# Kernel optimization log

Hardware: AMD Instinct MI355X
Metric: run time of the kernel (lower is better)

Reference implementation:

```python
import jax, jax.numpy as jnp
import numpy as np

B, L, R, D, K, H = 512, 10, 2048, 256, 20, 128
VOCAB, GEO_V, GEO_D = 30000, 1000, 64

def _l2norm(x):
    # F.normalize(p=2, dim=-1): x / max(||x||, eps)
    return x / jnp.maximum(jnp.linalg.norm(x, axis=-1, keepdims=True), 1e-12)

def setup_inputs() -> dict:
    key = jax.random.key(0)
    ks = jax.random.split(key, 20)
    emb = 0.02 * jax.random.normal(ks[0], (VOCAB, D), jnp.float32)
    emb = emb.at[0].set(0.0)  # padding_idx=0 row is zero
    inp = {
        'text_left': jax.random.randint(ks[1], (B, L), 0, VOCAB),
        'text_right': jax.random.randint(ks[2], (B, R), 0, VOCAB),
        'location_left': jax.random.randint(ks[3], (B, 2), 0, GEO_V),
        'distance': jax.random.uniform(ks[4], (B,), jnp.float32),
        'emb': emb,
        'attn_w': 0.05 * jax.random.normal(ks[5], (D,), jnp.float32),
        'w_m0': 0.1 * jax.random.normal(ks[6], (K, H), jnp.float32),
        'b_m0': jnp.zeros((H,), jnp.float32),
        'w_m1': 0.1 * jax.random.normal(ks[7], (H, H), jnp.float32),
        'b_m1': jnp.zeros((H,), jnp.float32),
        'w_m2': 0.1 * jax.random.normal(ks[8], (H, 1), jnp.float32),
        'b_m2': jnp.zeros((1,), jnp.float32),
        'out_w': 0.5 * jax.random.normal(ks[9], (1, 1), jnp.float32),
        'out_b': jnp.zeros((1,), jnp.float32),
        'lat_tab': 0.05 * jax.random.normal(ks[10], (GEO_V, GEO_D), jnp.float32),
        'lon_tab': 0.05 * jax.random.normal(ks[11], (GEO_V, GEO_D), jnp.float32),
        'w3': 0.05 * jax.random.normal(ks[12], (D, 10), jnp.float32),
        'b3': jnp.zeros((10,), jnp.float32),
        'w5': 0.05 * jax.random.normal(ks[13], (GEO_D, 32), jnp.float32),
        'b5': jnp.zeros((32,), jnp.float32),
        'w4': 0.05 * jax.random.normal(ks[14], (164, 2), jnp.float32),
        'b4': jnp.zeros((2,), jnp.float32),
    }
    return inp

def reference(text_left, text_right, location_left, distance, emb, attn_w,
              w_m0, b_m0, w_m1, b_m1, w_m2, b_m2, out_w, out_b,
              lat_tab, lon_tab, w3, b3, w5, b5, w4, b4):
    # ---- no_grad block in the original ----
    mask_query = text_left == 0  # mask_value = 0
    embed_query = emb[text_left]            # [B,L,D]
    embed_doc = emb[text_right]             # [B,R,D]
    matching = jnp.einsum('bld,brd->blr', _l2norm(embed_query), _l2norm(embed_doc))
    topk = jax.lax.top_k(matching, K)[0]    # [B,L,K], sorted descending
    logits = jnp.einsum('bld,d->bl', embed_query, attn_w)
    logits = jnp.where(mask_query, -jnp.inf, logits)
    attn = jax.nn.softmax(logits, axis=-1)  # [B,L]
    h = jnp.tanh(topk @ w_m0 + b_m0)
    h = jnp.tanh(h @ w_m1 + b_m1)
    h = jnp.tanh(h @ w_m2 + b_m2)[..., 0]   # [B,L]
    x = jnp.einsum('bl,bl->b', h, attn)[:, None]  # [B,1]
    x = jnp.tanh(x @ out_w + out_b)         # out layer (tanh)
    x = jax.lax.stop_gradient(x)
    embed_query = jax.lax.stop_gradient(embed_query)
    # ---- trainable geo/weighting branch ----
    lat = lat_tab[location_left[:, 0]] @ w5 + b5   # [B,32]
    lon = lon_tab[location_left[:, 1]] @ w5 + b5   # [B,32]
    q1 = (embed_query @ w3 + b3).reshape(embed_query.shape[0], -1)  # [B,100]
    w = jnp.concatenate([q1, lat, lon], axis=-1) @ w4 + b4          # [B,2]
    x_all = jnp.concatenate([x, distance[:, None]], axis=1)         # [B,2]
    pred = jnp.sum(w * x_all, axis=1, keepdims=True)                # [B,1]
    return pred
```

## Files before the change

### kernel.cpp

```cpp
#include <hip/hip_runtime.h>
#include <hip/hip_fp16.h>
#include <math.h>

#define BB 512
#define LL 10
#define RR 2048
#define DD 256
#define KK 20
#define HH 128
#define NVOCAB 30000
#define GEOD 64

#define FP8_SCALE   64.0f
#define FP8_DESCALE (1.0f / 4096.0f)

#define EMB8_BYTES (NVOCAB * DD)
#define BLOB1_OFF  EMB8_BYTES
#define BLOB2_OFF  (BLOB1_OFF + 8192)
#define W3T_OFF    (BLOB2_OFF + 32768)
#define W5T_OFF    (W3T_OFF + 10240)

typedef __attribute__((ext_vector_type(2))) long long llx2;
typedef __attribute__((ext_vector_type(4))) float f32x4;
typedef __attribute__((ext_vector_type(8))) short bf16x8;

static __device__ inline unsigned short f2bf(float f) {
    unsigned u = __float_as_uint(f);
    unsigned r = (u + 0x7fff + ((u >> 16) & 1)) >> 16;
    return (unsigned short)r;
}

__global__ __launch_bounds__(256) void pre_kernel(
    const float* __restrict__ emb,
    const float* __restrict__ w_m0, const float* __restrict__ w_m1,
    const float* __restrict__ w3,   const float* __restrict__ w5,
    unsigned char* __restrict__ emb8,
    unsigned short* __restrict__ blob1, unsigned short* __restrict__ blob2,
    float* __restrict__ w3T, float* __restrict__ w5T)
{
    if (blockIdx.x < 7500) {
        int row  = blockIdx.x * 4 + (threadIdx.x >> 6);
        int lane = threadIdx.x & 63;
        int e0 = ((lane >> 1) & 7) * 32 + (lane >> 4) * 8 + (lane & 1) * 4;
        float4 v = *(const float4*)(emb + (size_t)row * DD + e0);
        float ssq = v.x * v.x + v.y * v.y + v.z * v.z + v.w * v.w;
        #pragma unroll
        for (int off = 32; off; off >>= 1) ssq += __shfl_xor(ssq, off);
        float s = FP8_SCALE / fmaxf(sqrtf(ssq), 1e-12f);
        unsigned pk = 0;
        pk = (unsigned)__builtin_amdgcn_cvt_pk_fp8_f32(v.x * s, v.y * s, (int)pk, false);
        pk = (unsigned)__builtin_amdgcn_cvt_pk_fp8_f32(v.z * s, v.w * s, (int)pk, true);
        ((unsigned*)(emb8 + (size_t)row * DD))[lane] = pk;
    } else {
        int i = (blockIdx.x - 7500) * 256 + threadIdx.x;
        if (i < 4096) {
            int t = i >> 9, ln = (i >> 3) & 63, tt = i & 7;
            int n = t * 16 + (ln & 15), k = (ln >> 4) * 8 + tt;
            blob1[i] = (k < KK) ? f2bf(w_m0[k * HH + n]) : (unsigned short)0;
        } else if (i < 4096 + 16384) {
            int i2 = i - 4096;
            int ks = i2 >> 12, rem = i2 & 4095;
            int t = rem >> 9, ln = (rem >> 3) & 63, tt = rem & 7;
            int n = t * 16 + (ln & 15), k = ks * 32 + (ln >> 4) * 8 + tt;
            blob2[i2] = f2bf(w_m1[k * HH + n]);
        } else if (i < 4096 + 16384 + 2560) {
            int i3 = i - (4096 + 16384);
            int j = i3 >> 8, d = i3 & 255;
            w3T[i3] = w3[d * 10 + j];
        } else if (i < 4096 + 16384 + 2560 + 2048) {
            int i4 = i - (4096 + 16384 + 2560);
            int c = i4 >> 6, d = i4 & 63;
            w5T[i4] = w5[d * 32 + c];
        }
    }
}

static __device__ inline unsigned wave_umax_u32(unsigned x)
{
    unsigned t;
    t = (unsigned)__builtin_amdgcn_update_dpp((int)x, (int)x, 0x111, 0xF, 0xF, false); x = x > t ? x : t;
    t = (unsigned)__builtin_amdgcn_update_dpp((int)x, (int)x, 0x112, 0xF, 0xF, false); x = x > t ? x : t;
    t = (unsigned)__builtin_amdgcn_update_dpp((int)x, (int)x, 0x114, 0xF, 0xF, false); x = x > t ? x : t;
    t = (unsigned)__builtin_amdgcn_update_dpp((int)x, (int)x, 0x118, 0xF, 0xF, false); x = x > t ? x : t;
    t = (unsigned)__builtin_amdgcn_update_dpp((int)x, (int)x, 0x142, 0xF, 0xF, false); x = x > t ? x : t;
    t = (unsigned)__builtin_amdgcn_update_dpp((int)x, (int)x, 0x143, 0xF, 0xF, false); x = x > t ? x : t;
    return (unsigned)__builtin_amdgcn_readlane((int)x, 63);
}

static __device__ inline void build_top2(const unsigned short* __restrict__ row,
                                         int lane, unsigned extmask,
                                         unsigned& k1, unsigned& k2)
{
    unsigned m1 = 0u, m2 = 0u;
    #pragma unroll
    for (int k = 0; k < 32; ++k) {
        int j = lane + 64 * k;
        unsigned key = ((unsigned)row[j] << 16) | (unsigned)(2047 - j);
        key = ((extmask >> k) & 1u) ? 0u : key;
        unsigned mn = m1 < key ? m1 : key;
        m1 = m1 > key ? m1 : key;
        m2 = m2 > mn ? m2 : mn;
    }
    k1 = m1; k2 = m2;
}

__global__ __launch_bounds__(512, 4) void fused_kernel(
    const int*   __restrict__ text_left,
    const int*   __restrict__ text_right,
    const int*   __restrict__ loc_left,
    const float* __restrict__ distance,
    const float* __restrict__ emb,
    const float* __restrict__ attn_w,
    const float* __restrict__ b_m0, const float* __restrict__ b_m1,
    const float* __restrict__ w_m2, const float* __restrict__ b_m2,
    const float* __restrict__ out_w, const float* __restrict__ out_b,
    const float* __restrict__ lat_tab, const float* __restrict__ lon_tab,
    const float* __restrict__ b3, const float* __restrict__ b5,
    const float* __restrict__ w4, const float* __restrict__ b4,
    const unsigned char*  __restrict__ emb8,
    const unsigned short* __restrict__ blob1,
    const unsigned short* __restrict__ blob2,
    const float* __restrict__ w3T, const float* __restrict__ w5T,
    float*       __restrict__ out)
{
    __shared__ __align__(16) unsigned char arena[32768];
    __shared__ __align__(16) unsigned short s_keys[LL][RR];
    __shared__ float s_logit[LL];
    __shared__ float s_h[16];
    __shared__ float s_feat[164];

    unsigned short* s_h1   = (unsigned short*)arena;
    float*          s_topk = (float*)(arena + 4096);

    const int b    = blockIdx.x;
    const int tid  = threadIdx.x;
    const int lane = tid & 63;
    const int wid  = tid >> 6;
    const int m15  = lane & 15, q = lane >> 4;

    {
        llx2 afr[4];
        {
            int qidx = (m15 < LL) ? text_left[b * LL + m15] : 0;
            const unsigned char* ap = emb8 + (size_t)qidx * DD + q * 64;
            #pragma unroll
            for (int s = 0; s < 4; ++s) afr[s] = *(const llx2*)(ap + s * 16);
        }
        const int* trb = text_right + b * RR;
        const int T0 = wid * 16;
        const int r0 = lane >> 4;
        const int c  = lane & 15;

        unsigned char* stg = arena + wid * 4096;

        int  I[4];
        llx2 R[4];

        auto LOADI = [&](int t) {
            const int* p = trb + (T0 + t) * 16 + r0;
            I[0] = p[0]; I[1] = p[4]; I[2] = p[8]; I[3] = p[12];
        };
        auto LOADR = [&]() {
            #pragma unroll
            for (int j = 0; j < 4; ++j)
                R[j] = *(const llx2*)(emb8 + (size_t)I[j] * DD + (c << 4));
        };
        auto STORE = [&]() {
            #pragma unroll
            for (int j = 0; j < 4; ++j) {
                int r = j * 4 + r0;
                *(llx2*)(stg + r * 256 + ((c ^ r) << 4)) = R[j];
            }
        };
        auto COMPUTE = [&](int t) {
            llx2 bf[4];
            #pragma unroll
            for (int s = 0; s < 4; ++s)
                bf[s] = *(const llx2*)(stg + m15 * 256 + (((q * 4 + s) ^ m15) << 4));
            f32x4 acc = {0.f, 0.f, 0.f, 0.f};
            #pragma unroll
            for (int s = 0; s < 4; ++s) {
                acc = __builtin_amdgcn_mfma_f32_16x16x32_fp8_fp8(afr[s][0], bf[s][0], acc, 0, 0, 0);
                acc = __builtin_amdgcn_mfma_f32_16x16x32_fp8_fp8(afr[s][1], bf[s][1], acc, 0, 0, 0);
            }
            int n0 = (T0 + t) * 16;
            #pragma unroll
            for (int v = 0; v < 4; ++v) {
                int m = q * 4 + v;
                if (m < LL) {
                    float sc = acc[v] * FP8_DESCALE;
                    unsigned hb = (unsigned)__half_as_ushort(__float2half(sc));
                    unsigned ok = hb ^ ((hb & 0x8000u) ? 0xFFFFu : 0x8000u);
                    s_keys[m][n0 + m15] = (unsigned short)ok;
                }
            }
        };

        LOADI(0); LOADR(); LOADI(1);
        #pragma unroll 1
        for (int t = 0; t < 16; ++t) {
            STORE();
            if (t < 15) {
                LOADR();
                if (t < 14) LOADI(t + 2);
            }
            COMPUTE(t);
        }
    }
    __syncthreads();

    {
        int row = tid >> 5, col = tid & 31;
        if (row >= LL || col >= KK) s_topk[row * 32 + col] = 0.f;
    }

    {
        auto TOPK_ROW = [&](int l) {
            const unsigned short* krow = &s_keys[l][0];
            unsigned extmask = 0u, k1, k2;
            build_top2(krow, lane, extmask, k1, k2);
            #pragma unroll 1
            for (int it = 0; it < KK; ++it) {
                unsigned bmk = wave_umax_u32(k1);
                if (k1 == bmk) {
                    unsigned o16 = bmk >> 16;
                    unsigned hbv = (o16 & 0x8000u) ? (o16 & 0x7FFFu) : (o16 ^ 0xFFFFu);
                    s_topk[l * 32 + it] = __half2float(__ushort_as_half((unsigned short)hbv));
                    int j = 2047 - (int)(bmk & 0xFFFFu);
                    extmask |= 1u << (j >> 6);
                    k1 = k2; k2 = 0u;
                }
                if (__any(k1 == 0u)) {
                    if (k1 == 0u) build_top2(krow, lane, extmask, k1, k2);
                }
            }
        };
        TOPK_ROW(wid);
        if (wid >= 6) {
            TOPK_ROW(wid + 2);
        } else if (wid == 4) {
            const float4 aw = *(const float4*)(attn_w + lane * 4);
            for (int l = 0; l < LL; ++l) {
                int v = text_left[b * LL + l];
                float4 qv = *(const float4*)(emb + (size_t)v * DD + lane * 4);
                float d = qv.x * aw.x + qv.y * aw.y + qv.z * aw.z + qv.w * aw.w;
                #pragma unroll
                for (int off = 32; off; off >>= 1) d += __shfl_xor(d, off);
                if (lane == 0) s_logit[l] = (v == 0) ? -INFINITY : d;
            }
        } else if (wid == 5) {
            int c = lane & 31, which = lane >> 5;
            int v = loc_left[b * 2 + which];
            const float* tab = which ? lon_tab : lat_tab;
            const float4* tr = (const float4*)(tab + (size_t)v * GEOD);
            const float4* wr = (const float4*)(w5T + c * GEOD);
            float a = b5[c];
            #pragma unroll
            for (int d4 = 0; d4 < 16; ++d4) {
                float4 tv = tr[d4], wv = wr[d4];
                a += tv.x * wv.x + tv.y * wv.y + tv.z * wv.z + tv.w * wv.w;
            }
            s_feat[100 + which * 32 + c] = a;
        } else if (wid == 2 || wid == 3) {
            int p = (wid - 2) * 64 + lane;
            if (p < 100) {
                int l = p / 10, j = p % 10;
                int v = text_left[b * LL + l];
                const float4* qr = (const float4*)(emb + (size_t)v * DD);
                const float4* wr = (const float4*)(w3T + j * DD);
                float a = b3[j];
                #pragma unroll 8
                for (int d4 = 0; d4 < 64; ++d4) {
                    float4 qv = qr[d4], wv = wr[d4];
                    a += qv.x * wv.x + qv.y * wv.y + qv.z * wv.z + qv.w * wv.w;
                }
                s_feat[p] = a;
            }
        }
    }
    __syncthreads();

    if (wid == 0) {
        float tv[8];
        *(float4*)(tv)     = *(const float4*)(&s_topk[m15 * 32 + q * 8]);
        *(float4*)(tv + 4) = *(const float4*)(&s_topk[m15 * 32 + q * 8 + 4]);
        bf16x8 a1;
        #pragma unroll
        for (int t = 0; t < 8; ++t) a1[t] = (short)f2bf(tv[t]);
        f32x4 acc1[8];
        #pragma unroll
        for (int t = 0; t < 8; ++t) {
            bf16x8 b1 = *(const bf16x8*)(blob1 + t * 512 + lane * 8);
            f32x4 z = {0.f, 0.f, 0.f, 0.f};
            acc1[t] = __builtin_amdgcn_mfma_f32_16x16x32_bf16(a1, b1, z, 0, 0, 0);
        }
        #pragma unroll
        for (int t = 0; t < 8; ++t) {
            int c = t * 16 + m15;
            float bb0 = b_m0[c];
            #pragma unroll
            for (int v = 0; v < 4; ++v) {
                int m = q * 4 + v;
                float h = tanhf(acc1[t][v] + bb0);
                s_h1[m * 128 + (((c >> 3) ^ m) << 3) + (c & 7)] = f2bf(h);
            }
        }
        f32x4 acc2[8];
        #pragma unroll
        for (int t = 0; t < 8; ++t) acc2[t] = (f32x4){0.f, 0.f, 0.f, 0.f};
        #pragma unroll
        for (int ks = 0; ks < 4; ++ks) {
            bf16x8 a2 = *(const bf16x8*)(s_h1 + m15 * 128 + (((ks * 4 + q) ^ m15) << 3));
            #pragma unroll
            for (int t = 0; t < 8; ++t) {
                bf16x8 b2 = *(const bf16x8*)(blob2 + (ks * 8 + t) * 512 + lane * 8);
                acc2[t] = __builtin_amdgcn_mfma_f32_16x16x32_bf16(a2, b2, acc2[t], 0, 0, 0);
            }
        }
        float part[4] = {0.f, 0.f, 0.f, 0.f};
        #pragma unroll
        for (int t = 0; t < 8; ++t) {
            int c = t * 16 + m15;
            float bb1 = b_m1[c];
            float wm2 = w_m2[c];
            #pragma unroll
            for (int v = 0; v < 4; ++v)
                part[v] += tanhf(acc2[t][v] + bb1) * wm2;
        }
        #pragma unroll
        for (int v = 0; v < 4; ++v) {
            #pragma unroll
            for (int off = 1; off < 16; off <<= 1) part[v] += __shfl_xor(part[v], off);
        }
        if (m15 == 0) {
            #pragma unroll
            for (int v = 0; v < 4; ++v) {
                int m = q * 4 + v;
                if (m < LL) s_h[m] = tanhf(part[v] + b_m2[0]);
            }
        }
        float w0p = 0.f, w1p = 0.f;
        #pragma unroll
        for (int i = lane; i < 164; i += 64) {
            float f = s_feat[i];
            w0p += f * w4[i * 2 + 0];
            w1p += f * w4[i * 2 + 1];
        }
        #pragma unroll
        for (int off = 32; off; off >>= 1) {
            w0p += __shfl_xor(w0p, off);
            w1p += __shfl_xor(w1p, off);
        }
        if (lane == 0) {
            float mx = -INFINITY;
            #pragma unroll
            for (int l = 0; l < LL; ++l) mx = fmaxf(mx, s_logit[l]);
            float ex[LL];
            float sum = 0.f;
            #pragma unroll
            for (int l = 0; l < LL; ++l) { ex[l] = expf(s_logit[l] - mx); sum += ex[l]; }
            float x = 0.f;
            #pragma unroll
            for (int l = 0; l < LL; ++l) x += s_h[l] * (ex[l] / sum);
            float xo = tanhf(x * out_w[0] + out_b[0]);
            out[b] = (w0p + b4[0]) * xo + (w1p + b4[1]) * distance[b];
        }
    }
}

extern "C" void kernel_launch(void* const* d_in, const int* in_sizes, int n_in,
                              void* d_out, int out_size, void* d_ws, size_t ws_size,
                              hipStream_t stream) {
    const int*   text_left  = (const int*)  d_in[0];
    const int*   text_right = (const int*)  d_in[1];
    const int*   loc_left   = (const int*)  d_in[2];
    const float* distance   = (const float*)d_in[3];
    const float* emb        = (const float*)d_in[4];
    const float* attn_w     = (const float*)d_in[5];
    const float* w_m0       = (const float*)d_in[6];
    const float* b_m0       = (const float*)d_in[7];
    const float* w_m1       = (const float*)d_in[8];
    const float* b_m1       = (const float*)d_in[9];
    const float* w_m2       = (const float*)d_in[10];
    const float* b_m2       = (const float*)d_in[11];
    const float* out_w      = (const float*)d_in[12];
    const float* out_b      = (const float*)d_in[13];
    const float* lat_tab    = (const float*)d_in[14];
    const float* lon_tab    = (const float*)d_in[15];
    const float* w3         = (const float*)d_in[16];
    const float* b3         = (const float*)d_in[17];
    const float* w5         = (const float*)d_in[18];
    const float* b5         = (const float*)d_in[19];
    const float* w4         = (const float*)d_in[20];
    const float* b4         = (const float*)d_in[21];

    unsigned char*  ws    = (unsigned char*)d_ws;
    unsigned char*  emb8  = ws;
    unsigned short* blob1 = (unsigned short*)(ws + BLOB1_OFF);
    unsigned short* blob2 = (unsigned short*)(ws + BLOB2_OFF);
    float*          w3T   = (float*)(ws + W3T_OFF);
    float*          w5T   = (float*)(ws + W5T_OFF);
    float*          out   = (float*)d_out;

    pre_kernel<<<7598, 256, 0, stream>>>(emb, w_m0, w_m1, w3, w5,
                                         emb8, blob1, blob2, w3T, w5T);

    fused_kernel<<<BB, 512, 0, stream>>>(
        text_left, text_right, loc_left, distance, emb, attn_w,
        b_m0, b_m1, w_m2, b_m2, out_w, out_b,
        lat_tab, lon_tab, b3, b5, w4, b4,
        emb8, blob1, blob2, w3T, w5T, out);
}
```

Baseline: 57.58 us.

## Replace shared-memory key buffer with register-resident hierarchical top-k merge

Each wave now keeps its match scores in registers and tracks a running top-2 per row while computing. It then extracts a local top-20 per 16-lane group using shuffles, and a second stage merges 8x20 candidates per row from a small shared buffer. This removes the 40KB s_keys shared array and the full 2048-wide rescans, which should cut LDS traffic and raise occupancy. In exchange it uses more registers (savek, k1/k2 arrays) and adds an extra merge stage, and the side-branch work is redistributed across waves.

```diff
diff --git a/kernel.cpp b/kernel.cpp
--- a/kernel.cpp
+++ b/kernel.cpp
@@ -87,21 +87,14 @@
     return (unsigned)__builtin_amdgcn_readlane((int)x, 63);
 }
 
-static __device__ inline void build_top2(const unsigned short* __restrict__ row,
-                                         int lane, unsigned extmask,
-                                         unsigned& k1, unsigned& k2)
+static __device__ inline unsigned grp16_umax(unsigned x)
 {
-    unsigned m1 = 0u, m2 = 0u;
-    #pragma unroll
-    for (int k = 0; k < 32; ++k) {
-        int j = lane + 64 * k;
-        unsigned key = ((unsigned)row[j] << 16) | (unsigned)(2047 - j);
-        key = ((extmask >> k) & 1u) ? 0u : key;
-        unsigned mn = m1 < key ? m1 : key;
-        m1 = m1 > key ? m1 : key;
-        m2 = m2 > mn ? m2 : mn;
-    }
-    k1 = m1; k2 = m2;
+    unsigned t;
+    t = (unsigned)__shfl_xor((int)x, 1); x = x > t ? x : t;
+    t = (unsigned)__shfl_xor((int)x, 2); x = x > t ? x : t;
+    t = (unsigned)__shfl_xor((int)x, 4); x = x > t ? x : t;
+    t = (unsigned)__shfl_xor((int)x, 8); x = x > t ? x : t;
+    return x;
 }
 
 __global__ __launch_bounds__(512, 4) void fused_kernel(
@@ -124,13 +117,12 @@
     float*       __restrict__ out)
 {
     __shared__ __align__(16) unsigned char arena[32768];
-    __shared__ __align__(16) unsigned short s_keys[LL][RR];
+    __shared__ unsigned s_merge[LL][160];
+    __shared__ __align__(16) float s_topkf[16 * 32];
+    __shared__ __align__(16) unsigned short s_h1[16 * 128];
     __shared__ float s_logit[LL];
     __shared__ float s_h[16];
     __shared__ float s_feat[164];
-
-    unsigned short* s_h1   = (unsigned short*)arena;
-    float*          s_topk = (float*)(arena + 4096);
 
     const int b    = blockIdx.x;
     const int tid  = threadIdx.x;
@@ -138,6 +130,10 @@
     const int wid  = tid >> 6;
     const int m15  = lane & 15, q = lane >> 4;
 
+    unsigned savek[4][8];
+    unsigned k1[4] = {0u, 0u, 0u, 0u};
+    unsigned k2[4] = {0u, 0u, 0u, 0u};
+    const int T0 = wid * 16;
     {
         llx2 afr[4];
         {
@@ -147,10 +143,8 @@
             for (int s = 0; s < 4; ++s) afr[s] = *(const llx2*)(ap + s * 16);
         }
         const int* trb = text_right + b * RR;
-        const int T0 = wid * 16;
         const int r0 = lane >> 4;
         const int c  = lane & 15;
-
         unsigned char* stg = arena + wid * 4096;
 
         int  I[4];
@@ -172,118 +166,166 @@
                 *(llx2*)(stg + r * 256 + ((c ^ r) << 4)) = R[j];
             }
         };
-        auto COMPUTE = [&](int t) {
-            llx2 bf[4];
-            #pragma unroll
-            for (int s = 0; s < 4; ++s)
-                bf[s] = *(const llx2*)(stg + m15 * 256 + (((q * 4 + s) ^ m15) << 4));
-            f32x4 acc = {0.f, 0.f, 0.f, 0.f};
-            #pragma unroll
-            for (int s = 0; s < 4; ++s) {
-                acc = __builtin_amdgcn_mfma_f32_16x16x32_fp8_fp8(afr[s][0], bf[s][0], acc, 0, 0, 0);
-                acc = __builtin_amdgcn_mfma_f32_16x16x32_fp8_fp8(afr[s][1], bf[s][1], acc, 0, 0, 0);
-            }
-            int n0 = (T0 + t) * 16;
-            #pragma unroll
-            for (int v = 0; v < 4; ++v) {
-                int m = q * 4 + v;
-                if (m < LL) {
-                    float sc = acc[v] * FP8_DESCALE;
-                    unsigned hb = (unsigned)__half_as_ushort(__float2half(sc));
-                    unsigned ok = hb ^ ((hb & 0x8000u) ? 0xFFFFu : 0x8000u);
-                    s_keys[m][n0 + m15] = (unsigned short)ok;
+
+#define COMPT(T) { \
+        llx2 bf0 = *(const llx2*)(stg + m15 * 256 + (((q * 4 + 0) ^ m15) << 4)); \
+        llx2 bf1 = *(const llx2*)(stg + m15 * 256 + (((q * 4 + 1) ^ m15) << 4)); \
+        llx2 bf2 = *(const llx2*)(stg + m15 * 256 + (((q * 4 + 2) ^ m15) << 4)); \
+        llx2 bf3 = *(const llx2*)(stg + m15 * 256 + (((q * 4 + 3) ^ m15) << 4)); \
+        f32x4 acc = {0.f, 0.f, 0.f, 0.f}; \
+        acc = __builtin_amdgcn_mfma_f32_16x16x32_fp8_fp8(afr[0][0], bf0[0], acc, 0, 0, 0); \
+        acc = __builtin_amdgcn_mfma_f32_16x16x32_fp8_fp8(afr[0][1], bf0[1], acc, 0, 0, 0); \
+        acc = __builtin_amdgcn_mfma_f32_16x16x32_fp8_fp8(afr[1][0], bf1[0], acc, 0, 0, 0); \
+        acc = __builtin_amdgcn_mfma_f32_16x16x32_fp8_fp8(afr[1][1], bf1[1], acc, 0, 0, 0); \
+        acc = __builtin_amdgcn_mfma_f32_16x16x32_fp8_fp8(afr[2][0], bf2[0], acc, 0, 0, 0); \
+        acc = __builtin_amdgcn_mfma_f32_16x16x32_fp8_fp8(afr[2][1], bf2[1], acc, 0, 0, 0); \
+        acc = __builtin_amdgcn_mfma_f32_16x16x32_fp8_fp8(afr[3][0], bf3[0], acc, 0, 0, 0); \
+        acc = __builtin_amdgcn_mfma_f32_16x16x32_fp8_fp8(afr[3][1], bf3[1], acc, 0, 0, 0); \
+        _Pragma("unroll") \
+        for (int v = 0; v < 4; ++v) { \
+            float sc_ = acc[v] * FP8_DESCALE; \
+            unsigned hb_ = (unsigned)__half_as_ushort(__float2half(sc_)); \
+            unsigned ok_ = hb_ ^ ((hb_ & 0x8000u) ? 0xFFFFu : 0x8000u); \
+            if ((T) & 1) savek[v][(T) >> 1] |= ok_ << 16; \
+            else         savek[v][(T) >> 1]  = ok_; \
+            unsigned key_ = (ok_ << 16) | (2047u - (unsigned)(((T0 + (T)) << 4) + m15)); \
+            key_ = ((q * 4 + v) < LL) ? key_ : 0u; \
+            unsigned mn_ = k1[v] < key_ ? k1[v] : key_; \
+            k1[v] = k1[v] > key_ ? k1[v] : key_; \
+            k2[v] = k2[v] > mn_ ? k2[v] : mn_; \
+        } }
+
+#define TILE(T) { STORE(); if ((T) < 15) { LOADR(); } if ((T) < 14) { LOADI((T) + 2); } COMPT(T); }
+
+        LOADI(0); LOADR(); LOADI(1);
+        TILE(0)  TILE(1)  TILE(2)  TILE(3)
+        TILE(4)  TILE(5)  TILE(6)  TILE(7)
+        TILE(8)  TILE(9)  TILE(10) TILE(11)
+        TILE(12) TILE(13) TILE(14) TILE(15)
+#undef TILE
+#undef COMPT
+    }
+
+    {
+        #pragma unroll
+        for (int v = 0; v < 4; ++v) {
+            const int m = q * 4 + v;
+            if (m < LL) {
+                unsigned k1v = k1[v], k2v = k2[v];
+                unsigned last = 0xFFFFFFFFu;
+                #pragma unroll 1
+                for (int it = 0; it < KK; ++it) {
+                    unsigned bmk = grp16_umax(k1v);
+                    if (k1v == bmk) {
+                        s_merge[m][wid * 20 + it] = bmk;
+                        k1v = k2v; k2v = 0u;
+                    }
+                    last = bmk;
+                    if (k1v == 0u) {
+                        unsigned m1 = 0u, m2 = 0u;
+                        #pragma unroll
+                        for (int t = 0; t < 16; ++t) {
+                            unsigned ok = (t & 1) ? (savek[v][t >> 1] >> 16)
+                                                  : (savek[v][t >> 1] & 0xFFFFu);
+                            unsigned key = (ok << 16) | (2047u - (unsigned)(((T0 + t) << 4) + m15));
+                            key = (key < last) ? key : 0u;
+                            unsigned mn = m1 < key ? m1 : key;
+                            m1 = m1 > key ? m1 : key;
+                            m2 = m2 > mn ? m2 : mn;
+                        }
+                        k1v = m1; k2v = m2;
+                    }
                 }
             }
-        };
-
-        LOADI(0); LOADR(); LOADI(1);
-        #pragma unroll 1
-        for (int t = 0; t < 16; ++t) {
-            STORE();
-            if (t < 15) {
-                LOADR();
-                if (t < 14) LOADI(t + 2);
-            }
-            COMPUTE(t);
         }
     }
     __syncthreads();
 
     {
         int row = tid >> 5, col = tid & 31;
-        if (row >= LL || col >= KK) s_topk[row * 32 + col] = 0.f;
-    }
-
-    {
-        auto TOPK_ROW = [&](int l) {
-            const unsigned short* krow = &s_keys[l][0];
-            unsigned extmask = 0u, k1, k2;
-            build_top2(krow, lane, extmask, k1, k2);
+        if (row >= LL || col >= KK) s_topkf[row * 32 + col] = 0.f;
+    }
+    if (wid < 5) {
+        #pragma unroll 1
+        for (int rr = 0; rr < 2; ++rr) {
+            int m = wid + rr * 5;
+            unsigned s0 = s_merge[m][lane];
+            unsigned s1 = s_merge[m][lane + 64];
+            unsigned s2 = (lane < 32) ? s_merge[m][lane + 128] : 0u;
+            unsigned m1 = s0 > s1 ? s0 : s1;
+            unsigned m2 = s0 > s1 ? s1 : s0;
+            unsigned mn = m1 < s2 ? m1 : s2;
+            m1 = m1 > s2 ? m1 : s2;
+            m2 = m2 > mn ? m2 : mn;
+            unsigned last = 0xFFFFFFFFu;
             #pragma unroll 1
             for (int it = 0; it < KK; ++it) {
-                unsigned bmk = wave_umax_u32(k1);
-                if (k1 == bmk) {
+                unsigned bmk = wave_umax_u32(m1);
+                if (m1 == bmk) {
                     unsigned o16 = bmk >> 16;
                     unsigned hbv = (o16 & 0x8000u) ? (o16 & 0x7FFFu) : (o16 ^ 0xFFFFu);
-                    s_topk[l * 32 + it] = __half2float(__ushort_as_half((unsigned short)hbv));
-                    int j = 2047 - (int)(bmk & 0xFFFFu);
-                    extmask |= 1u << (j >> 6);
-                    k1 = k2; k2 = 0u;
+                    s_topkf[m * 32 + it] = __half2float(__ushort_as_half((unsigned short)hbv));
+                    m1 = m2; m2 = 0u;
                 }
-                if (__any(k1 == 0u)) {
-                    if (k1 == 0u) build_top2(krow, lane, extmask, k1, k2);
+                last = bmk;
+                if (__any(m1 == 0u)) {
+                    if (m1 == 0u) {
+                        unsigned a0 = (s0 < last) ? s0 : 0u;
+                        unsigned a1 = (s1 < last) ? s1 : 0u;
+                        unsigned a2 = (s2 < last) ? s2 : 0u;
+                        m1 = a0 > a1 ? a0 : a1;
+                        m2 = a0 > a1 ? a1 : a0;
+                        unsigned mn2 = m1 < a2 ? m1 : a2;
+                        m1 = m1 > a2 ? m1 : a2;
+                        m2 = m2 > mn2 ? m2 : mn2;
+                    }
                 }
             }
-        };
-        TOPK_ROW(wid);
-        if (wid >= 6) {
-            TOPK_ROW(wid + 2);
-        } else if (wid == 4) {
-            const float4 aw = *(const float4*)(attn_w + lane * 4);
-            for (int l = 0; l < LL; ++l) {
-                int v = text_left[b * LL + l];
-                float4 qv = *(const float4*)(emb + (size_t)v * DD + lane * 4);
-                float d = qv.x * aw.x + qv.y * aw.y + qv.z * aw.z + qv.w * aw.w;
-                #pragma unroll
-                for (int off = 32; off; off >>= 1) d += __shfl_xor(d, off);
-                if (lane == 0) s_logit[l] = (v == 0) ? -INFINITY : d;
-            }
-        } else if (wid == 5) {
-            int c = lane & 31, which = lane >> 5;
-            int v = loc_left[b * 2 + which];
-            const float* tab = which ? lon_tab : lat_tab;
-            const float4* tr = (const float4*)(tab + (size_t)v * GEOD);
-            const float4* wr = (const float4*)(w5T + c * GEOD);
-            float a = b5[c];
-            #pragma unroll
-            for (int d4 = 0; d4 < 16; ++d4) {
-                float4 tv = tr[d4], wv = wr[d4];
-                a += tv.x * wv.x + tv.y * wv.y + tv.z * wv.z + tv.w * wv.w;
-            }
-            s_feat[100 + which * 32 + c] = a;
-        } else if (wid == 2 || wid == 3) {
-            int p = (wid - 2) * 64 + lane;
-            if (p < 100) {
-                int l = p / 10, j = p % 10;
-                int v = text_left[b * LL + l];
-                const float4* qr = (const float4*)(emb + (size_t)v * DD);
-                const float4* wr = (const float4*)(w3T + j * DD);
-                float a = b3[j];
-                #pragma unroll 8
-                for (int d4 = 0; d4 < 64; ++d4) {
-                    float4 qv = qr[d4], wv = wr[d4];
-                    a += qv.x * wv.x + qv.y * wv.y + qv.z * wv.z + qv.w * wv.w;
-                }
-                s_feat[p] = a;
-            }
+        }
+    } else if (wid == 5) {
+        const float4 aw = *(const float4*)(attn_w + lane * 4);
+        for (int l = 0; l < LL; ++l) {
+            int v = text_left[b * LL + l];
+            float4 qv = *(const float4*)(emb + (size_t)v * DD + lane * 4);
+            float d = qv.x * aw.x + qv.y * aw.y + qv.z * aw.z + qv.w * aw.w;
+            #pragma unroll
+            for (int off = 32; off; off >>= 1) d += __shfl_xor(d, off);
+            if (lane == 0) s_logit[l] = (v == 0) ? -INFINITY : d;
+        }
+        int c = lane & 31, which = lane >> 5;
+        int v = loc_left[b * 2 + which];
+        const float* tab = which ? lon_tab : lat_tab;
+        const float4* tr = (const float4*)(tab + (size_t)v * GEOD);
+        const float4* wr = (const float4*)(w5T + c * GEOD);
+        float a = b5[c];
+        #pragma unroll
+        for (int d4 = 0; d4 < 16; ++d4) {
+            float4 tv = tr[d4], wv = wr[d4];
+            a += tv.x * wv.x + tv.y * wv.y + tv.z * wv.z + tv.w * wv.w;
+        }
+        s_feat[100 + which * 32 + c] = a;
+    } else {
+        int p = (wid - 6) * 64 + lane;
+        if (p < 100) {
+            int l = p / 10, j = p % 10;
+            int v = text_left[b * LL + l];
+            const float4* qr = (const float4*)(emb + (size_t)v * DD);
+            const float4* wr = (const float4*)(w3T + j * DD);
+            float a = b3[j];
+            #pragma unroll 8
+            for (int d4 = 0; d4 < 64; ++d4) {
+                float4 qv = qr[d4], wv = wr[d4];
+                a += qv.x * wv.x + qv.y * wv.y + qv.z * wv.z + qv.w * wv.w;
+            }
+            s_feat[p] = a;
         }
     }
     __syncthreads();
 
     if (wid == 0) {
         float tv[8];
-        *(float4*)(tv)     = *(const float4*)(&s_topk[m15 * 32 + q * 8]);
-        *(float4*)(tv + 4) = *(const float4*)(&s_topk[m15 * 32 + q * 8 + 4]);
+        *(float4*)(tv)     = *(const float4*)(&s_topkf[m15 * 32 + q * 8]);
+        *(float4*)(tv + 4) = *(const float4*)(&s_topkf[m15 * 32 + q * 8 + 4]);
         bf16x8 a1;
         #pragma unroll
         for (int t = 0; t < 8; ++t) a1[t] = (short)f2bf(tv[t]);
```

Measured after the change: 92.64 us. 1.61x slower.

## Split MLP tail across all waves and use nontemporal loads for gathers

Applied to the files above, without the earlier changes.

The per-block MLP (topk -> 128 -> 128 -> 1) previously ran entirely on wave 0. Now each of the 8 waves computes one 16-column tile of each layer, with partial sums combined through a new shared array and extra block barriers. The text_right index loads and fp8 embedding gathers are also switched to nontemporal loads to reduce cache pollution. The split adds two __syncthreads, and the nontemporal hint may hurt reuse of embedding rows shared across blocks.

```diff
diff --git a/kernel.cpp b/kernel.cpp
--- a/kernel.cpp
+++ b/kernel.cpp
@@ -125,6 +125,7 @@
 {
     __shared__ __align__(16) unsigned char arena[32768];
     __shared__ __align__(16) unsigned short s_keys[LL][RR];
+    __shared__ float s_part[8][16];
     __shared__ float s_logit[LL];
     __shared__ float s_h[16];
     __shared__ float s_feat[164];
@@ -158,12 +159,16 @@
 
         auto LOADI = [&](int t) {
             const int* p = trb + (T0 + t) * 16 + r0;
-            I[0] = p[0]; I[1] = p[4]; I[2] = p[8]; I[3] = p[12];
+            I[0] = __builtin_nontemporal_load(p);
+            I[1] = __builtin_nontemporal_load(p + 4);
+            I[2] = __builtin_nontemporal_load(p + 8);
+            I[3] = __builtin_nontemporal_load(p + 12);
         };
         auto LOADR = [&]() {
             #pragma unroll
             for (int j = 0; j < 4; ++j)
-                R[j] = *(const llx2*)(emb8 + (size_t)I[j] * DD + (c << 4));
+                R[j] = __builtin_nontemporal_load(
+                    (const llx2*)(emb8 + (size_t)I[j] * DD + (c << 4)));
         };
         auto STORE = [&]() {
             #pragma unroll
@@ -280,64 +285,60 @@
     }
     __syncthreads();
 
-    if (wid == 0) {
+    {
         float tv[8];
         *(float4*)(tv)     = *(const float4*)(&s_topk[m15 * 32 + q * 8]);
         *(float4*)(tv + 4) = *(const float4*)(&s_topk[m15 * 32 + q * 8 + 4]);
         bf16x8 a1;
         #pragma unroll
         for (int t = 0; t < 8; ++t) a1[t] = (short)f2bf(tv[t]);
-        f32x4 acc1[8];
-        #pragma unroll
-        for (int t = 0; t < 8; ++t) {
-            bf16x8 b1 = *(const bf16x8*)(blob1 + t * 512 + lane * 8);
+        {
+            bf16x8 b1 = *(const bf16x8*)(blob1 + wid * 512 + lane * 8);
             f32x4 z = {0.f, 0.f, 0.f, 0.f};
-            acc1[t] = __builtin_amdgcn_mfma_f32_16x16x32_bf16(a1, b1, z, 0, 0, 0);
-        }
-        #pragma unroll
-        for (int t = 0; t < 8; ++t) {
-            int c = t * 16 + m15;
+            f32x4 acc1 = __builtin_amdgcn_mfma_f32_16x16x32_bf16(a1, b1, z, 0, 0, 0);
+            int c = wid * 16 + m15;
             float bb0 = b_m0[c];
             #pragma unroll
             for (int v = 0; v < 4; ++v) {
                 int m = q * 4 + v;
-                float h = tanhf(acc1[t][v] + bb0);
+                float h = tanhf(acc1[v] + bb0);
                 s_h1[m * 128 + (((c >> 3) ^ m) << 3) + (c & 7)] = f2bf(h);
             }
         }
-        f32x4 acc2[8];
-        #pragma unroll
-        for (int t = 0; t < 8; ++t) acc2[t] = (f32x4){0.f, 0.f, 0.f, 0.f};
-        #pragma unroll
-        for (int ks = 0; ks < 4; ++ks) {
-            bf16x8 a2 = *(const bf16x8*)(s_h1 + m15 * 128 + (((ks * 4 + q) ^ m15) << 3));
-            #pragma unroll
-            for (int t = 0; t < 8; ++t) {
-                bf16x8 b2 = *(const bf16x8*)(blob2 + (ks * 8 + t) * 512 + lane * 8);
-                acc2[t] = __builtin_amdgcn_mfma_f32_16x16x32_bf16(a2, b2, acc2[t], 0, 0, 0);
-            }
-        }
-        float part[4] = {0.f, 0.f, 0.f, 0.f};
-        #pragma unroll
-        for (int t = 0; t < 8; ++t) {
-            int c = t * 16 + m15;
+        __syncthreads();
+        {
+            f32x4 acc2 = {0.f, 0.f, 0.f, 0.f};
+            #pragma unroll
+            for (int ks = 0; ks < 4; ++ks) {
+                bf16x8 a2 = *(const bf16x8*)(s_h1 + m15 * 128 + (((ks * 4 + q) ^ m15) << 3));
+                bf16x8 b2 = *(const bf16x8*)(blob2 + (ks * 8 + wid) * 512 + lane * 8);
+                acc2 = __builtin_amdgcn_mfma_f32_16x16x32_bf16(a2, b2, acc2, 0, 0, 0);
+            }
+            int c = wid * 16 + m15;
             float bb1 = b_m1[c];
             float wm2 = w_m2[c];
-            #pragma unroll
-            for (int v = 0; v < 4; ++v)
-                part[v] += tanhf(acc2[t][v] + bb1) * wm2;
-        }
-        #pragma unroll
-        for (int v = 0; v < 4; ++v) {
-            #pragma unroll
-            for (int off = 1; off < 16; off <<= 1) part[v] += __shfl_xor(part[v], off);
-        }
-        if (m15 == 0) {
+            float part[4];
+            #pragma unroll
+            for (int v = 0; v < 4; ++v) part[v] = tanhf(acc2[v] + bb1) * wm2;
             #pragma unroll
             for (int v = 0; v < 4; ++v) {
-                int m = q * 4 + v;
-                if (m < LL) s_h[m] = tanhf(part[v] + b_m2[0]);
-            }
+                #pragma unroll
+                for (int off = 1; off < 16; off <<= 1) part[v] += __shfl_xor(part[v], off);
+            }
+            if (m15 == 0) {
+                #pragma unroll
+                for (int v = 0; v < 4; ++v) s_part[wid][q * 4 + v] = part[v];
+            }
+        }
+    }
+    __syncthreads();
+
+    if (wid == 0) {
+        if (lane < LL) {
+            float a = 0.f;
+            #pragma unroll
+            for (int w = 0; w < 8; ++w) a += s_part[w][lane];
+            s_h[lane] = tanhf(a + b_m2[0]);
         }
         float w0p = 0.f, w1p = 0.f;
         #pragma unroll
```

New measurement: 64.92 us. 12.7% more time.

## Counting-sort doc token ids per block to improve embedding gather locality

Applied to the files above, without the earlier changes.

Before the fp8 MFMA matching loop, each block bucket-sorts its 2048 document token ids by id>>7 into a shared-memory array, using atomics and a Hillis-Steele prefix scan. The sorted ids drive the gather, and warps interleave over 16-row tiles. The goal is to make concurrent embedding-row fetches hit nearby memory for better L2 and TLB locality. Top-k over the matching scores does not depend on column order, so results are unchanged. The cost is several extra barriers, 2048 shared atomics and extra shared memory per block.

```diff
diff --git a/kernel.cpp b/kernel.cpp
--- a/kernel.cpp
+++ b/kernel.cpp
@@ -125,6 +125,7 @@
 {
     __shared__ __align__(16) unsigned char arena[32768];
     __shared__ __align__(16) unsigned short s_keys[LL][RR];
+    __shared__ __align__(8) unsigned short s_docs[RR];
     __shared__ float s_logit[LL];
     __shared__ float s_h[16];
     __shared__ float s_feat[164];
@@ -139,6 +140,38 @@
     const int m15  = lane & 15, q = lane >> 4;
 
     {
+        unsigned* s_cnt = (unsigned*)arena;
+        unsigned* s_off = (unsigned*)(arena + 1024);
+        if (tid < 256) s_cnt[tid] = 0u;
+        __syncthreads();
+        const int* trb = text_right + b * RR;
+        int dv[4];
+        #pragma unroll
+        for (int i = 0; i < 4; ++i) {
+            dv[i] = trb[tid * 4 + i];
+            atomicAdd(&s_cnt[dv[i] >> 7], 1u);
+        }
+        __syncthreads();
+        if (tid < 256) s_off[tid + 1] = s_cnt[tid];
+        if (tid == 0) s_off[0] = 0u;
+        __syncthreads();
+        #pragma unroll 1
+        for (int st = 1; st < 256; st <<= 1) {
+            unsigned v = 0u;
+            if (tid < 256 && tid + 1 > st) v = s_off[tid + 1 - st];
+            __syncthreads();
+            if (tid < 256 && tid + 1 > st) s_off[tid + 1] += v;
+            __syncthreads();
+        }
+        #pragma unroll
+        for (int i = 0; i < 4; ++i) {
+            unsigned p = atomicAdd(&s_off[dv[i] >> 7], 1u);
+            s_docs[p] = (unsigned short)dv[i];
+        }
+        __syncthreads();
+    }
+
+    {
         llx2 afr[4];
         {
             int qidx = (m15 < LL) ? text_left[b * LL + m15] : 0;
@@ -146,8 +179,6 @@
             #pragma unroll
             for (int s = 0; s < 4; ++s) afr[s] = *(const llx2*)(ap + s * 16);
         }
-        const int* trb = text_right + b * RR;
-        const int T0 = wid * 16;
         const int r0 = lane >> 4;
         const int c  = lane & 15;
 
@@ -156,8 +187,8 @@
         int  I[4];
         llx2 R[4];
 
-        auto LOADI = [&](int t) {
-            const int* p = trb + (T0 + t) * 16 + r0;
+        auto LOADI = [&](int i) {
+            const unsigned short* p = s_docs + (wid + 8 * i) * 16 + r0;
             I[0] = p[0]; I[1] = p[4]; I[2] = p[8]; I[3] = p[12];
         };
         auto LOADR = [&]() {
@@ -172,7 +203,7 @@
                 *(llx2*)(stg + r * 256 + ((c ^ r) << 4)) = R[j];
             }
         };
-        auto COMPUTE = [&](int t) {
+        auto COMPUTE = [&](int i) {
             llx2 bf[4];
             #pragma unroll
             for (int s = 0; s < 4; ++s)
@@ -183,7 +214,7 @@
                 acc = __builtin_amdgcn_mfma_f32_16x16x32_fp8_fp8(afr[s][0], bf[s][0], acc, 0, 0, 0);
                 acc = __builtin_amdgcn_mfma_f32_16x16x32_fp8_fp8(afr[s][1], bf[s][1], acc, 0, 0, 0);
             }
-            int n0 = (T0 + t) * 16;
+            int n0 = (wid + 8 * i) * 16;
             #pragma unroll
             for (int v = 0; v < 4; ++v) {
                 int m = q * 4 + v;
```

New measurement: 55.46 us. 3.7% less time.
